# Kernel tuning notes

Measured on AMD Instinct MI355X. Metric: run time of the kernel, lower is better.

## Reference

```python
import jax, jax.numpy as jnp
import numpy as np

B, N, F = 8, 2048, 64
H, LAT = 256, 64
K1, K2 = N // 2, N // 4  # DiffPool keeps nodes//2 per stage


def _adj_mm(A, x):
    # A: [N,M] (shared) or [B,N,M] (per-sample); x: [B,M,F]
    if A.ndim == 2:
        return jnp.einsum('nm,bmf->bnf', A, x)
    return jnp.einsum('bnm,bmf->bnf', A, x)


def _gcn(x, A, W, b, act=None):
    # spektral GCNConv: act(A @ (X W) + b)
    h = _adj_mm(A, x @ W) + b
    return act(h) if act is not None else h


def _diffpool(x, A, K_emb, K_pool):
    # spektral DiffPool (linear embedding activation, softmax selection)
    z = _adj_mm(A, x @ K_emb)                               # [B,N,C]
    s = jax.nn.softmax(_adj_mm(A, x @ K_pool), axis=-1)     # [B,N,K]
    x_pool = jnp.einsum('bnk,bnc->bkc', s, z)               # S^T Z
    AS = _adj_mm(A, s)                                       # [B,N,K]
    A_pool = jnp.einsum('bnk,bnl->bkl', s, AS)              # S^T A S
    return x_pool, A_pool, s


def setup_inputs() -> dict:
    key = jax.random.key(0)
    ks = jax.random.split(key, 24)

    def glorot(k, shape):
        return (jax.random.normal(k, shape) * jnp.sqrt(2.0 / (shape[0] + shape[1]))).astype(jnp.float32)

    # symmetric sparse-ish adjacency with self loops, GCN-normalized (keeps activations stable)
    mask = (jax.random.uniform(ks[0], (N, N)) < 0.01).astype(jnp.float32)
    A = jnp.minimum(jnp.maximum(mask, mask.T) + jnp.eye(N, dtype=jnp.float32), 1.0)
    dinv = 1.0 / jnp.sqrt(jnp.sum(A, axis=-1))
    adj = A * dinv[:, None] * dinv[None, :]

    return {
        'x': jax.random.normal(ks[1], (B, N, F), dtype=jnp.float32),
        'eps': jax.random.normal(ks[2], (B, K2, LAT), dtype=jnp.float32),
        'adj': adj,
        'We1': glorot(ks[3], (F, H)), 'be1': jnp.zeros((H,), jnp.float32),
        'Kemb1': glorot(ks[4], (H, H)), 'Kpool1': glorot(ks[5], (H, K1)),
        'We2': glorot(ks[6], (H, H)), 'be2': jnp.zeros((H,), jnp.float32),
        'Kemb2': glorot(ks[7], (H, H)), 'Kpool2': glorot(ks[8], (H, K2)),
        'We3': glorot(ks[9], (H, 2 * LAT)), 'be3': jnp.zeros((2 * LAT,), jnp.float32),
        'Wd0': glorot(ks[10], (LAT, H)), 'bd0': jnp.zeros((H,), jnp.float32),
        'Wd1': glorot(ks[11], (H, H)), 'bd1': jnp.zeros((H,), jnp.float32),
        'Wd2': glorot(ks[12], (H, H)), 'bd2': jnp.zeros((H,), jnp.float32),
        'Wdf': glorot(ks[13], (H, F)), 'bdf': jnp.zeros((F,), jnp.float32),
    }


def reference(x, eps, adj, We1, be1, Kemb1, Kpool1, We2, be2, Kemb2, Kpool2,
              We3, be3, Wd0, bd0, Wd1, bd1, Wd2, bd2, Wdf, bdf):
    A0 = adj
    # ---- encode ----
    h = _gcn(x, A0, We1, be1, jax.nn.relu)              # [B,N,H]
    h, A1, s1 = _diffpool(h, A0, Kemb1, Kpool1)          # [B,K1,H], [B,K1,K1], [B,N,K1]
    h = _gcn(h, A1, We2, be2, jax.nn.relu)
    h, A2, s2 = _diffpool(h, A1, Kemb2, Kpool2)          # [B,K2,H]
    h = _gcn(h, A2, We3, be3, None)                      # [B,K2,2*LAT]
    mean, log_var = jnp.split(h, 2, axis=-1)
    z = mean + jnp.exp(0.5 * log_var) * eps              # reparameterize
    # ---- decode ----
    d = _gcn(z, A2, Wd0, bd0, jax.nn.relu)
    d = jnp.einsum('bnk,bkc->bnc', s2, d)                # DiffUnpool: S @ x
    d = _gcn(d, A1, Wd1, bd1, jax.nn.relu)
    d = jnp.einsum('bnk,bkc->bnc', s1, d)
    d = _gcn(d, A0, Wd2, bd2, jax.nn.relu)
    out = _gcn(d, A0, Wdf, bdf, jax.nn.softplus)         # [B,N,F]
    return out, mean, log_var
```

## Files before the change

### kernel.cpp

```cpp
#include <hip/hip_runtime.h>
#include <math.h>

#define BATCH 8
typedef unsigned short US;

typedef __attribute__((ext_vector_type(8))) short short8;
typedef __attribute__((ext_vector_type(4))) float f32x4;

__device__ __forceinline__ US f2b(float f) {
  union { float f; unsigned u; } v; v.f = f;
  unsigned r = v.u + 0x7fffu + ((v.u >> 16) & 1u);
  return (US)(r >> 16);
}
__device__ __forceinline__ float b2f(US h) {
  union { unsigned u; float f; } v; v.u = ((unsigned)h) << 16;
  return v.f;
}

__device__ __forceinline__ void gload16(const US* g, US* l) {
  __builtin_amdgcn_global_load_lds(
      (const __attribute__((address_space(1))) unsigned int*)g,
      (__attribute__((address_space(3))) unsigned int*)l, 16, 0, 0);
}

__device__ __forceinline__ int lidx2(int r, int ko) {
  return r * 64 + ((((ko >> 3) ^ (r & 7)) << 3));
}

template <int TN, int ACT, int OUT, bool HASBIAS>
__global__ __launch_bounds__(256) void mm_k(
    const US* __restrict__ A, const US* __restrict__ B,
    const float* __restrict__ bias, void* __restrict__ Cv, void* __restrict__ Cv2,
    int M, int N, int K, int lda, long long sA, long long sB, long long sC,
    long long sC2, int gx, int gy) {
  constexpr int JF = TN / 32;
  __shared__ US As[128 * 64];
  __shared__ US Bs[TN * 64];

  const int nb = blockIdx.x;
  const int nb2 = (nb & 7) * (gx * gy) + (nb >> 3);
  const int bx = nb2 % gx;
  const int by = (nb2 / gx) % gy;
  const int b = nb2 / (gx * gy);

  A += (long long)b * sA;
  B += (long long)b * sB;
  const int m0 = by * 128, n0 = bx * TN;
  const int t = threadIdx.x, lane = t & 63, w = t >> 6;
  const int wm = (w >> 1) * 64, wn = (w & 1) * (TN / 2);
  const int l15 = lane & 15, lg = lane >> 4;
  const int lrow = lane >> 3;
  const int gcell = (((lane & 7) ^ lrow) << 3);

  f32x4 acc[4][JF];
#pragma unroll
  for (int i = 0; i < 4; ++i)
#pragma unroll
    for (int j = 0; j < JF; ++j) acc[i][j] = (f32x4){0.f, 0.f, 0.f, 0.f};

  for (int k0 = 0; k0 < K; k0 += 64) {
#pragma unroll
    for (int i = 0; i < 4; ++i) {
      const int g = w * 4 + i;
      gload16(A + (long long)(m0 + g * 8 + lrow) * lda + k0 + gcell, &As[g * 512]);
    }
#pragma unroll
    for (int i = 0; i < TN / 32; ++i) {
      const int g = w * (TN / 32) + i;
      gload16(B + (long long)(n0 + g * 8 + lrow) * K + k0 + gcell, &Bs[g * 512]);
    }
    __syncthreads();

#pragma unroll
    for (int kk = 0; kk < 2; ++kk) {
      const int ko = kk * 32 + lg * 8;
      short8 af[4], bf[JF];
#pragma unroll
      for (int i = 0; i < 4; ++i)
        af[i] = *(const short8*)&As[lidx2(wm + i * 16 + l15, ko)];
#pragma unroll
      for (int j = 0; j < JF; ++j)
        bf[j] = *(const short8*)&Bs[lidx2(wn + j * 16 + l15, ko)];
#pragma unroll
      for (int i = 0; i < 4; ++i)
#pragma unroll
        for (int j = 0; j < JF; ++j)
          acc[i][j] = __builtin_amdgcn_mfma_f32_16x16x32_bf16(af[i], bf[j],
                                                              acc[i][j], 0, 0, 0);
    }
    __syncthreads();
  }

  const long long cb = (long long)b * sC;
  const long long cb2 = (long long)b * sC2;
#pragma unroll
  for (int fj = 0; fj < JF; ++fj) {
    const int col = n0 + wn + fj * 16 + l15;
    const float bsv = HASBIAS ? bias[col] : 0.0f;
#pragma unroll
    for (int fi = 0; fi < 4; ++fi) {
      const int row0 = m0 + wm + fi * 16 + lg * 4;
      float v[4];
#pragma unroll
      for (int e = 0; e < 4; ++e) {
        float x = acc[fi][fj][e] + bsv;
        if (ACT == 1) x = fmaxf(x, 0.0f);
        if (ACT == 2) x = (x > 20.0f) ? x : log1pf(expf(x));
        v[e] = x;
      }
      if (OUT == 1 || OUT == 3) {
        ushort4 pk;
        pk.x = f2b(v[0]); pk.y = f2b(v[1]); pk.z = f2b(v[2]); pk.w = f2b(v[3]);
        US* c2 = (OUT == 3) ? (US*)Cv2 : (US*)Cv;
        *(ushort4*)&c2[cb2 + (long long)col * M + row0] = pk;
      }
      if (OUT == 0 || OUT == 3) {
#pragma unroll
        for (int e = 0; e < 4; ++e)
          ((US*)Cv)[cb + (long long)(row0 + e) * N + col] = f2b(v[e]);
      }
      if (OUT == 2) {
#pragma unroll
        for (int e = 0; e < 4; ++e)
          ((float*)Cv)[cb + (long long)(row0 + e) * N + col] = v[e];
      }
    }
  }
}

template <int OUT>
__global__ __launch_bounds__(512, 1) void mm256_k(
    const US* __restrict__ A, const US* __restrict__ B, void* __restrict__ Cv,
    void* __restrict__ Cv2, int M, int N, int K, int lda, long long sA,
    long long sB, long long sC, long long sC2, int gx, int gy) {
  __shared__ US lds[8][8192];

  const int nb = blockIdx.x;
  const int chunk = gx * gy;
  const int nb2 = (nb & 7) * chunk + (nb >> 3);
  const int bx = nb2 % gx;
  const int by = (nb2 / gx) % gy;
  const int b = nb2 / chunk;

  const int m0 = by * 256, n0 = bx * 256;
  const int tid = threadIdx.x;
  const int lane = tid & 63, w = tid >> 6;
  const int wr = w >> 2, wc = w & 3;
  const int l15 = lane & 15, lg = lane >> 4;

  const US* Ab = A + (long long)b * sA + (long long)m0 * lda;
  const US* Bb = B + (long long)b * sB + (long long)n0 * K;
  const int NT = K >> 6;

  auto stageH = [&](int H) {
    const int s = H >> 2, h = H & 3;
    const int ab = h & 1, kk = h >> 1;
    US* reg = &lds[ab * 4 + (s & 1) * 2 + kk][0];
    const US* src = ab ? Bb : Ab;
    const int ld = ab ? K : lda;
#pragma unroll
    for (int i = 0; i < 2; ++i) {
      const int rbase = (w * 2 + i) * 16;
      const int r = rbase + (lane >> 2);
      const int csrc = (lane & 3) ^ ((r >> 1) & 3);
      gload16(src + (long long)r * ld + s * 64 + kk * 32 + csrc * 8,
              reg + rbase * 32);
    }
  };

  f32x4 acc[8][4];
#pragma unroll
  for (int m = 0; m < 8; ++m)
#pragma unroll
    for (int j = 0; j < 4; ++j) acc[m][j] = (f32x4){0.f, 0.f, 0.f, 0.f};
  short8 a4[4], b4[4];

  for (int H = 0; H < 6; ++H) stageH(H);
  asm volatile("s_waitcnt vmcnt(4)" ::: "memory");
  __builtin_amdgcn_s_barrier();

#define PH(kk_, mh_, DOH, HV, VM, tt)                                          \
  {                                                                            \
    const US* Ar = &lds[((tt) & 1) * 2 + (kk_)][0];                            \
    const US* Br = &lds[4 + ((tt) & 1) * 2 + (kk_)][0];                        \
    _Pragma("unroll") for (int i = 0; i < 4; ++i) {                            \
      const int r = wr * 128 + (mh_) * 64 + i * 16 + l15;                      \
      a4[i] = *(const short8*)&Ar[r * 32 + ((lg ^ ((r >> 1) & 3)) << 3)];      \
    }                                                                          \
    if ((mh_) == 0) {                                                          \
      _Pragma("unroll") for (int j = 0; j < 4; ++j) {                          \
        const int rr = wc * 64 + j * 16 + l15;                                 \
        b4[j] = *(const short8*)&Br[rr * 32 + ((lg ^ ((rr >> 1) & 3)) << 3)];  \
      }                                                                        \
    }                                                                          \
    if (DOH) stageH(HV);                                                       \
    if ((VM) == 1) asm volatile("s_waitcnt vmcnt(4)" ::: "memory");            \
    if ((VM) == 2) asm volatile("s_waitcnt vmcnt(0)" ::: "memory");            \
    __builtin_amdgcn_s_barrier();                                              \
    __builtin_amdgcn_s_setprio(1);                                             \
    _Pragma("unroll") for (int i = 0; i < 4; ++i)                              \
      _Pragma("unroll") for (int j = 0; j < 4; ++j)                            \
        acc[(mh_) * 4 + i][j] = __builtin_amdgcn_mfma_f32_16x16x32_bf16(       \
            a4[i], b4[j], acc[(mh_) * 4 + i][j], 0, 0, 0);                     \
    __builtin_amdgcn_s_setprio(0);                                             \
    __builtin_amdgcn_s_barrier();                                              \
  }

  int t2 = 0;
  for (; t2 < NT - 2; ++t2) {
    PH(0, 0, true, 4 * t2 + 6, 0, t2)
    PH(0, 1, true, 4 * t2 + 7, 0, t2)
    PH(1, 0, true, 4 * t2 + 8, 0, t2)
    PH(1, 1, true, 4 * t2 + 9, 1, t2)
  }
  PH(0, 0, true, 4 * (NT - 2) + 6, 0, NT - 2)
  PH(0, 1, true, 4 * (NT - 2) + 7, 0, NT - 2)
  PH(1, 0, false, 0, 0, NT - 2)
  PH(1, 1, false, 0, 2, NT - 2)
  PH(0, 0, false, 0, 0, NT - 1)
  PH(0, 1, false, 0, 0, NT - 1)
  PH(1, 0, false, 0, 0, NT - 1)
  PH(1, 1, false, 0, 0, NT - 1)
#undef PH

  const long long cb = (long long)b * sC;
  const long long cb2 = (long long)b * sC2;
#pragma unroll
  for (int j = 0; j < 4; ++j) {
    const int col = n0 + wc * 64 + j * 16 + l15;
#pragma unroll
    for (int m = 0; m < 8; ++m) {
      const int row0 = m0 + wr * 128 + m * 16 + lg * 4;
      if (OUT == 1 || OUT == 3) {
        ushort4 pk;
        pk.x = f2b(acc[m][j][0]); pk.y = f2b(acc[m][j][1]);
        pk.z = f2b(acc[m][j][2]); pk.w = f2b(acc[m][j][3]);
        US* c2 = (OUT == 3) ? (US*)Cv2 : (US*)Cv;
        *(ushort4*)&c2[cb2 + (long long)col * M + row0] = pk;
      }
      if (OUT == 0 || OUT == 3) {
#pragma unroll
        for (int e = 0; e < 4; ++e)
          ((US*)Cv)[cb + (long long)(row0 + e) * N + col] = f2b(acc[m][j][e]);
      }
    }
  }
}

template <int ACT, int OUT, bool HASBIAS>
__global__ __launch_bounds__(256) void mm64_k(
    const US* __restrict__ A, const US* __restrict__ B,
    const float* __restrict__ bias, void* __restrict__ Cv,
    int M, int N, int K, int lda, long long sA, long long sB, long long sC,
    int gx, int gy) {
  __shared__ US As[4][4096];
  __shared__ US Bs[4][4096];

  const int nb = blockIdx.x;
  const int chunk = gx * gy;
  const int nb2 = (nb & 7) * chunk + (nb >> 3);
  const int bx = nb2 % gx;
  const int by = (nb2 / gx) % gy;
  const int b = nb2 / chunk;

  const int m0 = by * 64, n0 = bx * 64;
  const int tid = threadIdx.x;
  const int lane = tid & 63, w = tid >> 6;
  const int wr = w >> 1, wc = w & 1;
  const int l15 = lane & 15, lg = lane >> 4;
  const int lrow = lane >> 3;
  const int gcell = (((lane & 7) ^ lrow) << 3);

  const US* Ag = A + (long long)b * sA + (long long)m0 * lda;
  const US* Bg = B + (long long)b * sB + (long long)n0 * K;
  const int NT = K >> 6;

  auto stage = [&](int tt) {
    US* Ad = &As[tt & 3][0];
    US* Bd = &Bs[tt & 3][0];
    const int k0 = tt * 64;
#pragma unroll
    for (int i = 0; i < 2; ++i) {
      const int g = w * 2 + i;
      const int r = g * 8 + lrow;
      gload16(Ag + (long long)r * lda + k0 + gcell, Ad + g * 512);
      gload16(Bg + (long long)r * K + k0 + gcell, Bd + g * 512);
    }
  };

  f32x4 acc[2][2];
#pragma unroll
  for (int i = 0; i < 2; ++i)
#pragma unroll
    for (int j = 0; j < 2; ++j) acc[i][j] = (f32x4){0.f, 0.f, 0.f, 0.f};

  for (int i = 0; i < 3 && i < NT; ++i) stage(i);

  for (int t = 0; t < NT; ++t) {
    if (t + 3 < NT) stage(t + 3);
    const int rem = NT - 1 - t;
    if (rem >= 3) asm volatile("s_waitcnt vmcnt(12)" ::: "memory");
    else if (rem == 2) asm volatile("s_waitcnt vmcnt(8)" ::: "memory");
    else if (rem == 1) asm volatile("s_waitcnt vmcnt(4)" ::: "memory");
    else asm volatile("s_waitcnt vmcnt(0)" ::: "memory");
    __builtin_amdgcn_s_barrier();
    const US* Ad = &As[t & 3][0];
    const US* Bd = &Bs[t & 3][0];
#pragma unroll
    for (int kk = 0; kk < 2; ++kk) {
      const int ko = kk * 32 + lg * 8;
      short8 af[2], bf[2];
      af[0] = *(const short8*)&Ad[lidx2(wr * 32 + l15, ko)];
      af[1] = *(const short8*)&Ad[lidx2(wr * 32 + 16 + l15, ko)];
      bf[0] = *(const short8*)&Bd[lidx2(wc * 32 + l15, ko)];
      bf[1] = *(const short8*)&Bd[lidx2(wc * 32 + 16 + l15, ko)];
#pragma unroll
      for (int i = 0; i < 2; ++i)
#pragma unroll
        for (int j = 0; j < 2; ++j)
          acc[i][j] = __builtin_amdgcn_mfma_f32_16x16x32_bf16(af[i], bf[j],
                                                              acc[i][j], 0, 0, 0);
    }
    __builtin_amdgcn_s_barrier();
  }

  const long long cb = (long long)b * sC;
#pragma unroll
  for (int fj = 0; fj < 2; ++fj) {
    const int col = n0 + wc * 32 + fj * 16 + l15;
    const float bsv = HASBIAS ? bias[col] : 0.0f;
#pragma unroll
    for (int fi = 0; fi < 2; ++fi) {
      const int row0 = m0 + wr * 32 + fi * 16 + lg * 4;
      float v[4];
#pragma unroll
      for (int e = 0; e < 4; ++e) {
        float x = acc[fi][fj][e] + bsv;
        if (ACT == 1) x = fmaxf(x, 0.0f);
        if (ACT == 2) x = (x > 20.0f) ? x : log1pf(expf(x));
        v[e] = x;
      }
      if (OUT == 1) {
        ushort4 pk;
        pk.x = f2b(v[0]); pk.y = f2b(v[1]); pk.z = f2b(v[2]); pk.w = f2b(v[3]);
        *(ushort4*)&((US*)Cv)[cb + (long long)col * M + row0] = pk;
      } else if (OUT == 0) {
#pragma unroll
        for (int e = 0; e < 4; ++e)
          ((US*)Cv)[cb + (long long)(row0 + e) * N + col] = f2b(v[e]);
      } else {
#pragma unroll
        for (int e = 0; e < 4; ++e)
          ((float*)Cv)[cb + (long long)(row0 + e) * N + col] = v[e];
      }
    }
  }
}

template <int RPT>
__global__ __launch_bounds__(256) void sm_partial_k(
    const US* __restrict__ x, float* __restrict__ pm, float* __restrict__ ps,
    int R, int C, long long sB, int NS) {
  const int b = blockIdx.y, blk = blockIdx.x;
  const int cpr = C >> 3;
  const int t = threadIdx.x;
  const int cslot = t & (cpr - 1);
  const int rsub = t / cpr;
  const int nsub = 256 / cpr;
  const int rowsPerBlock = R / NS;
  const int r0 = blk * rowsPerBlock + rsub * RPT;
  const US* p = x + (long long)b * sB + (long long)r0 * C + cslot * 8;
  union { uint4 v; US s[8]; } buf[RPT];
#pragma unroll
  for (int i = 0; i < RPT; ++i) buf[i].v = *(const uint4*)(p + (long long)i * C);
  float M[8], S[8];
#pragma unroll
  for (int j = 0; j < 8; ++j) M[j] = b2f(buf[0].s[j]);
#pragma unroll
  for (int i = 1; i < RPT; ++i)
#pragma unroll
    for (int j = 0; j < 8; ++j) M[j] = fmaxf(M[j], b2f(buf[i].s[j]));
#pragma unroll
  for (int j = 0; j < 8; ++j) S[j] = 0.f;
#pragma unroll
  for (int i = 0; i < RPT; ++i)
#pragma unroll
    for (int j = 0; j < 8; ++j) S[j] += __expf(b2f(buf[i].s[j]) - M[j]);
  const long long pi = (long long)(b * NS + blk) * nsub + rsub;
  float* pmo = pm + pi * C + cslot * 8;
  float* pso = ps + pi * C + cslot * 8;
  *(float4*)pmo = make_float4(M[0], M[1], M[2], M[3]);
  *(float4*)(pmo + 4) = make_float4(M[4], M[5], M[6], M[7]);
  *(float4*)pso = make_float4(S[0], S[1], S[2], S[3]);
  *(float4*)(pso + 4) = make_float4(S[4], S[5], S[6], S[7]);
}

__global__ __launch_bounds__(256) void sm_combine_k(
    const float* __restrict__ pm, const float* __restrict__ ps,
    float* __restrict__ Mf, float* __restrict__ Sinv, int C, int NP) {
  const int b = blockIdx.x, t = threadIdx.x;
  const int cpr = C >> 3;
  if (t >= cpr) return;
  const int c = t * 8;
  const float* pmB = pm + (long long)b * NP * C + c;
  const float* psB = ps + (long long)b * NP * C + c;
  float M[8], S[8];
#pragma unroll
  for (int j = 0; j < 8; ++j) { M[j] = pmB[j]; S[j] = psB[j]; }
  for (int e = 1; e < NP; ++e) {
    const float* pme = pmB + (long long)e * C;
    const float* pse = psB + (long long)e * C;
#pragma unroll
    for (int j = 0; j < 8; ++j) {
      const float m2 = pme[j], s2 = pse[j];
      const float nm = fmaxf(M[j], m2);
      S[j] = S[j] * __expf(M[j] - nm) + s2 * __expf(m2 - nm);
      M[j] = nm;
    }
  }
#pragma unroll
  for (int j = 0; j < 8; ++j) {
    Mf[(long long)b * C + c + j] = M[j];
    Sinv[(long long)b * C + c + j] = 1.0f / S[j];
  }
}

template <int RPT>
__global__ __launch_bounds__(256) void sm_norm_k(
    US* __restrict__ x, const float* __restrict__ Mf,
    const float* __restrict__ Sinv, int R, int C, long long sB, int NS) {
  const int b = blockIdx.y, blk = blockIdx.x;
  const int cpr = C >> 3;
  const int t = threadIdx.x;
  const int cslot = t & (cpr - 1);
  const int rsub = t / cpr;
  const int rowsPerBlock = R / NS;
  const int r0 = blk * rowsPerBlock + rsub * RPT;
  US* p = x + (long long)b * sB + (long long)r0 * C + cslot * 8;
  float M[8], Si[8];
#pragma unroll
  for (int j = 0; j < 8; ++j) {
    M[j] = Mf[(long long)b * C + cslot * 8 + j];
    Si[j] = Sinv[(long long)b * C + cslot * 8 + j];
  }
#pragma unroll
  for (int i = 0; i < RPT; ++i) {
    union { uint4 v; US s[8]; } buf;
    buf.v = *(const uint4*)(p + (long long)i * C);
#pragma unroll
    for (int j = 0; j < 8; ++j)
      buf.s[j] = f2b(__expf(b2f(buf.s[j]) - M[j]) * Si[j]);
    *(uint4*)(p + (long long)i * C) = buf.v;
  }
}

__global__ __launch_bounds__(256) void trans_k(const float* __restrict__ src,
                                               US* __restrict__ dst, int R, int C,
                                               long long sIn, long long sOut) {
  __shared__ US L[64][65];
  const int b = blockIdx.z;
  const int r0 = blockIdx.y * 64, c0 = blockIdx.x * 64;
  const int t = threadIdx.x;
  const int lr = t >> 4, lc = (t & 15) * 4;
  const float* s = src + (long long)b * sIn;
#pragma unroll
  for (int i = 0; i < 4; ++i) {
    const int rr = r0 + lr + 16 * i;
    const float4 v = *(const float4*)&s[(long long)rr * C + c0 + lc];
    L[lr + 16 * i][lc + 0] = f2b(v.x);
    L[lr + 16 * i][lc + 1] = f2b(v.y);
    L[lr + 16 * i][lc + 2] = f2b(v.z);
    L[lr + 16 * i][lc + 3] = f2b(v.w);
  }
  __syncthreads();
#pragma unroll
  for (int i = 0; i < 4; ++i) {
    ushort4 o;
    o.x = L[lc + 0][lr + 16 * i];
    o.y = L[lc + 1][lr + 16 * i];
    o.z = L[lc + 2][lr + 16 * i];
    o.w = L[lc + 3][lr + 16 * i];
    *(ushort4*)&dst[(long long)b * sOut + (long long)(c0 + lr + 16 * i) * R + r0 + lc] = o;
  }
}

struct WT { const float* src; US* dst; int R, C, tileOff; };
struct WTab { WT e[11]; };

__global__ __launch_bounds__(256) void wtrans_k(WTab tab) {
  __shared__ US L[64][65];
  const int tile = blockIdx.x;
  int i = 0;
#pragma unroll
  for (int j = 1; j < 11; ++j)
    if (tab.e[j].tileOff <= tile) i = j;
  const WT w = tab.e[i];
  const int lt = tile - w.tileOff;
  const int tc = w.C / 64;
  const int r0 = (lt / tc) * 64, c0 = (lt % tc) * 64;
  const int t = threadIdx.x;
  const int lr = t >> 4, lc = (t & 15) * 4;
#pragma unroll
  for (int k = 0; k < 4; ++k) {
    const int rr = r0 + lr + 16 * k;
    const float4 v = *(const float4*)&w.src[(long long)rr * w.C + c0 + lc];
    L[lr + 16 * k][lc + 0] = f2b(v.x);
    L[lr + 16 * k][lc + 1] = f2b(v.y);
    L[lr + 16 * k][lc + 2] = f2b(v.z);
    L[lr + 16 * k][lc + 3] = f2b(v.w);
  }
  __syncthreads();
#pragma unroll
  for (int k = 0; k < 4; ++k) {
    ushort4 o;
    o.x = L[lc + 0][lr + 16 * k];
    o.y = L[lc + 1][lr + 16 * k];
    o.z = L[lc + 2][lr + 16 * k];
    o.w = L[lc + 3][lr + 16 * k];
    *(ushort4*)&w.dst[(long long)(c0 + lr + 16 * k) * w.R + r0 + lc] = o;
  }
}

__global__ __launch_bounds__(256) void f2b_k(const float* __restrict__ s,
                                             US* __restrict__ d, int n4) {
  const int i = blockIdx.x * 256 + threadIdx.x;
  if (i < n4) {
    const float4 v = ((const float4*)s)[i];
    ushort4 o;
    o.x = f2b(v.x); o.y = f2b(v.y); o.z = f2b(v.z); o.w = f2b(v.w);
    ((ushort4*)d)[i] = o;
  }
}

__global__ __launch_bounds__(256) void reparam_k(
    const float* __restrict__ h3, const float* __restrict__ eps,
    float* __restrict__ om, float* __restrict__ olv, US* __restrict__ z,
    int total) {
  const int i = blockIdx.x * 256 + threadIdx.x;
  if (i >= total) return;
  const int j = i & 63;
  const long long r = i >> 6;
  const float m = h3[r * 128 + j];
  const float lv = h3[r * 128 + 64 + j];
  om[i] = m;
  olv[i] = lv;
  z[i] = f2b(m + expf(0.5f * lv) * eps[i]);
}

static void mm(hipStream_t st, const US* A, const US* B, const float* bias,
               void* C, void* C2, int M, int N, int K, int lda, long long sA,
               long long sB, long long sC, long long sC2, int act, int outm,
               int tn) {
  const int gx = N / tn, gy = M / 128;
  dim3 g(gx * gy * BATCH), blk(256);
#define L(TN, ACT, OUT, HB) \
  mm_k<TN, ACT, OUT, HB><<<g, blk, 0, st>>>(A, B, bias, C, C2, M, N, K, lda, sA, sB, sC, sC2, gx, gy)
  if (tn == 64) {
    if (outm == 0) L(64, 0, 0, false);
    else if (outm == 1) L(64, 0, 1, false);
    else L(64, 2, 2, true);
  } else {
    if (outm == 0) {
      if (act == 1) L(128, 1, 0, true);
      else L(128, 0, 0, false);
    } else if (outm == 1) {
      if (act == 1) L(128, 1, 1, true);
      else L(128, 0, 1, false);
    } else if (outm == 2) L(128, 0, 2, true);
    else L(128, 0, 3, false);
  }
#undef L
}

static void mm256(hipStream_t st, const US* A, const US* B, void* C, void* C2,
                  int M, int N, int K, int lda, long long sA, long long sB,
                  long long sC, long long sC2, int outm) {
  const int gx = N / 256, gy = M / 256;
  dim3 g(gx * gy * BATCH), blk(512);
  if (outm == 0)
    mm256_k<0><<<g, blk, 0, st>>>(A, B, C, C2, M, N, K, lda, sA, sB, sC, sC2, gx, gy);
  else if (outm == 1)
    mm256_k<1><<<g, blk, 0, st>>>(A, B, C, C2, M, N, K, lda, sA, sB, sC, sC2, gx, gy);
  else
    mm256_k<3><<<g, blk, 0, st>>>(A, B, C, C2, M, N, K, lda, sA, sB, sC, sC2, gx, gy);
}

static void mm64(hipStream_t st, const US* A, const US* B, const float* bias,
                 void* C, int M, int N, int K, int lda, long long sA,
                 long long sB, long long sC, int act, int outm) {
  const int gx = N / 64, gy = M / 64;
  dim3 g(gx * gy * BATCH), blk(256);
  if (outm == 0)
    mm64_k<0, 0, false><<<g, blk, 0, st>>>(A, B, nullptr, C, M, N, K, lda, sA, sB, sC, gx, gy);
  else if (outm == 1)
    mm64_k<0, 1, false><<<g, blk, 0, st>>>(A, B, nullptr, C, M, N, K, lda, sA, sB, sC, gx, gy);
  else
    mm64_k<2, 2, true><<<g, blk, 0, st>>>(A, B, bias, C, M, N, K, lda, sA, sB, sC, gx, gy);
}

extern "C" void kernel_launch(void* const* d_in, const int* in_sizes, int n_in,
                              void* d_out, int out_size, void* d_ws, size_t ws_size,
                              hipStream_t stream) {
  const float* x      = (const float*)d_in[0];
  const float* eps    = (const float*)d_in[1];
  const float* adj    = (const float*)d_in[2];
  const float* We1    = (const float*)d_in[3];
  const float* be1    = (const float*)d_in[4];
  const float* Kemb1  = (const float*)d_in[5];
  const float* Kpool1 = (const float*)d_in[6];
  const float* We2    = (const float*)d_in[7];
  const float* be2    = (const float*)d_in[8];
  const float* Kemb2  = (const float*)d_in[9];
  const float* Kpool2 = (const float*)d_in[10];
  const float* We3    = (const float*)d_in[11];
  const float* be3    = (const float*)d_in[12];
  const float* Wd0    = (const float*)d_in[13];
  const float* bd0    = (const float*)d_in[14];
  const float* Wd1    = (const float*)d_in[15];
  const float* bd1    = (const float*)d_in[16];
  const float* Wd2    = (const float*)d_in[17];
  const float* bd2    = (const float*)d_in[18];
  const float* Wdf    = (const float*)d_in[19];
  const float* bdf    = (const float*)d_in[20];
  (void)in_sizes; (void)n_in; (void)ws_size; (void)out_size;

  float* out = (float*)d_out;
  float* out_mean = out + (long long)8 * 2048 * 64;
  float* out_lv = out_mean + (long long)8 * 512 * 64;

  char* base = (char*)d_ws;
  size_t off = 0;
  auto alloc = [&](size_t bytes) {
    char* p = base + off;
    off += (bytes + 255) & ~(size_t)255;
    return p;
  };
  US* adjb = (US*)alloc(2048LL * 2048 * 2);
  US* xT   = (US*)alloc(8LL * 64 * 2048 * 2);
  US* Y0   = (US*)alloc(8LL * 2048 * 64 * 2);
  US* h1T  = (US*)alloc(8LL * 256 * 2048 * 2);
  US* g1   = (US*)alloc(8LL * 2048 * 256 * 2);
  US* R1   = (US*)alloc(8LL * 2304 * 2048 * 2);
  US* AS1  = (US*)alloc(8LL * 2048 * 1024 * 2);
  US* P1o  = (US*)alloc(8LL * 1024 * 1280 * 2);
  US* t1T  = (US*)alloc(8LL * 256 * 1024 * 2);
  US* h2T  = (US*)alloc(8LL * 256 * 1024 * 2);
  US* g2   = (US*)alloc(8LL * 1024 * 256 * 2);
  US* R2   = (US*)alloc(8LL * 1280 * 1024 * 2);
  US* AS2  = (US*)alloc(8LL * 1024 * 512 * 2);
  US* P2o  = (US*)alloc(8LL * 512 * 768 * 2);
  US* t2T  = (US*)alloc(8LL * 128 * 512 * 2);
  float* h3f = (float*)alloc(8LL * 512 * 128 * 4);
  US* zlb  = (US*)alloc(8LL * 512 * 64 * 2);
  US* t3T  = (US*)alloc(8LL * 256 * 512 * 2);
  US* d0   = (US*)alloc(8LL * 512 * 256 * 2);
  US* t4T  = (US*)alloc(8LL * 256 * 512 * 2);
  US* d2   = (US*)alloc(8LL * 1024 * 256 * 2);
  US* t5T  = (US*)alloc(8LL * 256 * 1024 * 2);
  US* d4   = (US*)alloc(8LL * 2048 * 256 * 2);
  US* t6T  = (US*)alloc(8LL * 64 * 2048 * 2);
  float* pm   = (float*)alloc(8LL * 128 * 2048 * 4);
  float* ps   = (float*)alloc(8LL * 128 * 2048 * 4);
  float* Mf   = (float*)alloc(8LL * 2048 * 4);
  float* Sinv = (float*)alloc(8LL * 2048 * 4);
  US* We1T  = (US*)alloc(256 * 64 * 2);
  US* KpKe1 = (US*)alloc(1280 * 256 * 2);
  US* We2T  = (US*)alloc(256 * 256 * 2);
  US* KpKe2 = (US*)alloc(768 * 256 * 2);
  US* We3T  = (US*)alloc(128 * 256 * 2);
  US* Wd0T  = (US*)alloc(256 * 64 * 2);
  US* Wd1T  = (US*)alloc(256 * 256 * 2);
  US* Wd2T  = (US*)alloc(256 * 256 * 2);
  US* WdfT  = (US*)alloc(64 * 256 * 2);

  f2b_k<<<dim3(2048 * 2048 / 4 / 256), dim3(256), 0, stream>>>(adj, adjb, 2048 * 2048 / 4);
  trans_k<<<dim3(1, 32, 8), dim3(256), 0, stream>>>(x, xT, 2048, 64, 2048LL * 64,
                                                    64LL * 2048);
  {
    WTab tab;
    int toff = 0, i = 0;
    auto add = [&](const float* s, US* d, int R, int C) {
      tab.e[i++] = WT{s, d, R, C, toff};
      toff += (R / 64) * (C / 64);
    };
    add(We1, We1T, 64, 256);
    add(Kpool1, KpKe1, 256, 1024);
    add(Kemb1, KpKe1 + 1024 * 256, 256, 256);
    add(We2, We2T, 256, 256);
    add(Kpool2, KpKe2, 256, 512);
    add(Kemb2, KpKe2 + 512 * 256, 256, 256);
    add(We3, We3T, 256, 128);
    add(Wd0, Wd0T, 64, 256);
    add(Wd1, Wd1T, 256, 256);
    add(Wd2, Wd2T, 256, 256);
    add(Wdf, WdfT, 256, 64);
    wtrans_k<<<dim3(toff), dim3(256), 0, stream>>>(tab);
  }

  const long long SR1 = 2304LL * 2048, SR2 = 1280LL * 1024;
  US* s1T  = R1;
  US* B1   = R1 + 1024 * 2048;
  US* AS1T = R1 + 1280 * 2048;
  US* s2T  = R2;
  US* B2   = R2 + 512 * 1024;
  US* AS2T = R2 + 768 * 1024;
  US* A1c  = P1o + 256;
  US* A2c  = P2o + 256;

  mm64(stream, adjb, xT, nullptr, Y0, 2048, 64, 2048, 2048, 0, 64LL * 2048,
       2048LL * 64, 0, 0);
  mm(stream, Y0, We1T, be1, h1T, nullptr, 2048, 256, 64, 64, 2048LL * 64, 0, 0,
     256LL * 2048, 1, 1, 128);
  mm(stream, adjb, h1T, nullptr, g1, nullptr, 2048, 256, 2048, 2048, 0,
     256LL * 2048, 2048LL * 256, 0, 0, 0, 128);
  mm(stream, g1, KpKe1, nullptr, R1, nullptr, 2048, 1280, 256, 256, 2048LL * 256,
     0, 0, SR1, 0, 1, 128);
  sm_partial_k<8><<<dim3(128, 8), dim3(256), 0, stream>>>(s1T, pm, ps, 1024, 2048, SR1, 128);
  sm_combine_k<<<dim3(8), dim3(256), 0, stream>>>(pm, ps, Mf, Sinv, 2048, 128);
  sm_norm_k<8><<<dim3(128, 8), dim3(256), 0, stream>>>(s1T, Mf, Sinv, 1024, 2048, SR1, 128);
  mm256(stream, adjb, s1T, AS1, AS1T, 2048, 1024, 2048, 2048, 0, SR1,
        2048LL * 1024, SR1, 3);
  mm(stream, s1T, B1, nullptr, P1o, nullptr, 1024, 1280, 2048, 2048, SR1, SR1,
     1024LL * 1280, 0, 0, 0, 128);
  mm(stream, P1o, We2T, nullptr, t1T, nullptr, 1024, 256, 256, 1280, 1024LL * 1280,
     0, 0, 256LL * 1024, 0, 1, 128);
  mm(stream, A1c, t1T, be2, h2T, nullptr, 1024, 256, 1024, 1280, 1024LL * 1280,
     256LL * 1024, 0, 256LL * 1024, 1, 1, 128);
  mm(stream, A1c, h2T, nullptr, g2, nullptr, 1024, 256, 1024, 1280, 1024LL * 1280,
     256LL * 1024, 1024LL * 256, 0, 0, 0, 128);
  mm(stream, g2, KpKe2, nullptr, R2, nullptr, 1024, 768, 256, 256, 1024LL * 256,
     0, 0, SR2, 0, 1, 128);
  sm_partial_k<4><<<dim3(64, 8), dim3(256), 0, stream>>>(s2T, pm, ps, 512, 1024, SR2, 64);
  sm_combine_k<<<dim3(8), dim3(256), 0, stream>>>(pm, ps, Mf, Sinv, 1024, 128);
  sm_norm_k<4><<<dim3(64, 8), dim3(256), 0, stream>>>(s2T, Mf, Sinv, 512, 1024, SR2, 64);
  mm(stream, A1c, s2T, nullptr, AS2, AS2T, 1024, 512, 1024, 1280, 1024LL * 1280,
     SR2, 1024LL * 512, SR2, 0, 3, 128);
  mm(stream, s2T, B2, nullptr, P2o, nullptr, 512, 768, 1024, 1024, SR2, SR2,
     512LL * 768, 0, 0, 0, 128);
  mm(stream, P2o, We3T, nullptr, t2T, nullptr, 512, 128, 256, 768, 512LL * 768,
     0, 0, 128LL * 512, 0, 1, 128);
  mm(stream, A2c, t2T, be3, h3f, nullptr, 512, 128, 512, 768, 512LL * 768,
     128LL * 512, 512LL * 128, 0, 0, 2, 128);
  reparam_k<<<dim3(8 * 512 * 64 / 256), dim3(256), 0, stream>>>(h3f, eps, out_mean,
                                                                out_lv, zlb, 8 * 512 * 64);

  mm(stream, zlb, Wd0T, nullptr, t3T, nullptr, 512, 256, 64, 64, 512LL * 64, 0, 0,
     256LL * 512, 0, 1, 128);
  mm(stream, A2c, t3T, bd0, d0, nullptr, 512, 256, 512, 768, 512LL * 768,
     256LL * 512, 512LL * 256, 0, 1, 0, 128);
  mm(stream, d0, Wd1T, nullptr, t4T, nullptr, 512, 256, 256, 256, 512LL * 256, 0,
     0, 256LL * 512, 0, 1, 128);
  mm(stream, AS2, t4T, bd1, d2, nullptr, 1024, 256, 512, 512, 1024LL * 512,
     256LL * 512, 1024LL * 256, 0, 1, 0, 128);
  mm(stream, d2, Wd2T, nullptr, t5T, nullptr, 1024, 256, 256, 256, 1024LL * 256, 0,
     0, 256LL * 1024, 0, 1, 128);
  mm(stream, AS1, t5T, bd2, d4, nullptr, 2048, 256, 1024, 1024, 2048LL * 1024,
     256LL * 1024, 2048LL * 256, 0, 1, 0, 128);
  mm64(stream, d4, WdfT, nullptr, t6T, 2048, 64, 256, 256, 2048LL * 256, 0,
       64LL * 2048, 0, 1);
  mm64(stream, adjb, t6T, bdf, out, 2048, 64, 2048, 2048, 0, 64LL * 2048,
       2048LL * 64, 2, 2);
}
```

Baseline: 664.4 us.

## Double-buffer generic GEMM, trim barriers in 256 GEMM, route big GEMMs to it

The generic mm_k kernel gets double-buffered LDS staging, so the next K-tile's global-to-LDS loads are issued while MFMAs run on the current tile. The 256-tile pipelined kernel drops several per-phase barriers and keeps only those needed for buffer reuse. Two large GEMMs, the pooling projection and S^T·B, are moved from the 128-tile kernel to the 256-tile kernel. Double buffering doubles LDS use, which may lower occupancy, and removing barriers risks LDS read/write races if the remaining ones are not enough.

Result: slower. 714.9 us (+7.6%).

```diff
diff --git a/kernel.cpp b/kernel.cpp
--- a/kernel.cpp
+++ b/kernel.cpp
@@ -34,8 +34,8 @@
     int M, int N, int K, int lda, long long sA, long long sB, long long sC,
     long long sC2, int gx, int gy) {
   constexpr int JF = TN / 32;
-  __shared__ US As[128 * 64];
-  __shared__ US Bs[TN * 64];
+  __shared__ US As[2][128 * 64];
+  __shared__ US Bs[2][TN * 64];
 
   const int nb = blockIdx.x;
   const int nb2 = (nb & 7) * (gx * gy) + (nb >> 3);
@@ -52,35 +52,43 @@
   const int lrow = lane >> 3;
   const int gcell = (((lane & 7) ^ lrow) << 3);
 
-  f32x4 acc[4][JF];
-#pragma unroll
-  for (int i = 0; i < 4; ++i)
-#pragma unroll
-    for (int j = 0; j < JF; ++j) acc[i][j] = (f32x4){0.f, 0.f, 0.f, 0.f};
-
-  for (int k0 = 0; k0 < K; k0 += 64) {
+  auto stage = [&](int buf, int k0) {
 #pragma unroll
     for (int i = 0; i < 4; ++i) {
       const int g = w * 4 + i;
-      gload16(A + (long long)(m0 + g * 8 + lrow) * lda + k0 + gcell, &As[g * 512]);
+      gload16(A + (long long)(m0 + g * 8 + lrow) * lda + k0 + gcell,
+              &As[buf][g * 512]);
     }
 #pragma unroll
     for (int i = 0; i < TN / 32; ++i) {
       const int g = w * (TN / 32) + i;
-      gload16(B + (long long)(n0 + g * 8 + lrow) * K + k0 + gcell, &Bs[g * 512]);
-    }
-    __syncthreads();
-
+      gload16(B + (long long)(n0 + g * 8 + lrow) * K + k0 + gcell,
+              &Bs[buf][g * 512]);
+    }
+  };
+
+  f32x4 acc[4][JF];
+#pragma unroll
+  for (int i = 0; i < 4; ++i)
+#pragma unroll
+    for (int j = 0; j < JF; ++j) acc[i][j] = (f32x4){0.f, 0.f, 0.f, 0.f};
+
+  stage(0, 0);
+  __syncthreads();
+
+  int cur = 0;
+  for (int k0 = 0; k0 < K; k0 += 64) {
+    if (k0 + 64 < K) stage(cur ^ 1, k0 + 64);
 #pragma unroll
     for (int kk = 0; kk < 2; ++kk) {
       const int ko = kk * 32 + lg * 8;
       short8 af[4], bf[JF];
 #pragma unroll
       for (int i = 0; i < 4; ++i)
-        af[i] = *(const short8*)&As[lidx2(wm + i * 16 + l15, ko)];
+        af[i] = *(const short8*)&As[cur][lidx2(wm + i * 16 + l15, ko)];
 #pragma unroll
       for (int j = 0; j < JF; ++j)
-        bf[j] = *(const short8*)&Bs[lidx2(wn + j * 16 + l15, ko)];
+        bf[j] = *(const short8*)&Bs[cur][lidx2(wn + j * 16 + l15, ko)];
 #pragma unroll
       for (int i = 0; i < 4; ++i)
 #pragma unroll
@@ -88,7 +96,9 @@
           acc[i][j] = __builtin_amdgcn_mfma_f32_16x16x32_bf16(af[i], bf[j],
                                                               acc[i][j], 0, 0, 0);
     }
-    __syncthreads();
+    asm volatile("s_waitcnt vmcnt(0)" ::: "memory");
+    asm volatile("s_barrier" ::: "memory");
+    cur ^= 1;
   }
 
   const long long cb = (long long)b * sC;
@@ -177,9 +187,9 @@
 
   for (int H = 0; H < 6; ++H) stageH(H);
   asm volatile("s_waitcnt vmcnt(4)" ::: "memory");
-  __builtin_amdgcn_s_barrier();
-
-#define PH(kk_, mh_, DOH, HV, VM, tt)                                          \
+  asm volatile("s_barrier" ::: "memory");
+
+#define PH(kk_, mh_, DOH, HV, VM, PB, EB, tt)                                  \
   {                                                                            \
     const US* Ar = &lds[((tt) & 1) * 2 + (kk_)][0];                            \
     const US* Br = &lds[4 + ((tt) & 1) * 2 + (kk_)][0];                        \
@@ -196,31 +206,31 @@
     if (DOH) stageH(HV);                                                       \
     if ((VM) == 1) asm volatile("s_waitcnt vmcnt(4)" ::: "memory");            \
     if ((VM) == 2) asm volatile("s_waitcnt vmcnt(0)" ::: "memory");            \
-    __builtin_amdgcn_s_barrier();                                              \
+    if (PB) asm volatile("s_barrier" ::: "memory");                            \
     __builtin_amdgcn_s_setprio(1);                                             \
     _Pragma("unroll") for (int i = 0; i < 4; ++i)                              \
       _Pragma("unroll") for (int j = 0; j < 4; ++j)                            \
         acc[(mh_) * 4 + i][j] = __builtin_amdgcn_mfma_f32_16x16x32_bf16(       \
             a4[i], b4[j], acc[(mh_) * 4 + i][j], 0, 0, 0);                     \
     __builtin_amdgcn_s_setprio(0);                                             \
-    __builtin_amdgcn_s_barrier();                                              \
+    if (EB) asm volatile("s_barrier" ::: "memory");                            \
   }
 
   int t2 = 0;
   for (; t2 < NT - 2; ++t2) {
-    PH(0, 0, true, 4 * t2 + 6, 0, t2)
-    PH(0, 1, true, 4 * t2 + 7, 0, t2)
-    PH(1, 0, true, 4 * t2 + 8, 0, t2)
-    PH(1, 1, true, 4 * t2 + 9, 1, t2)
-  }
-  PH(0, 0, true, 4 * (NT - 2) + 6, 0, NT - 2)
-  PH(0, 1, true, 4 * (NT - 2) + 7, 0, NT - 2)
-  PH(1, 0, false, 0, 0, NT - 2)
-  PH(1, 1, false, 0, 2, NT - 2)
-  PH(0, 0, false, 0, 0, NT - 1)
-  PH(0, 1, false, 0, 0, NT - 1)
-  PH(1, 0, false, 0, 0, NT - 1)
-  PH(1, 1, false, 0, 0, NT - 1)
+    PH(0, 0, true, 4 * t2 + 6, 0, 0, 0, t2)
+    PH(0, 1, true, 4 * t2 + 7, 0, 0, 1, t2)
+    PH(1, 0, true, 4 * t2 + 8, 0, 0, 0, t2)
+    PH(1, 1, true, 4 * t2 + 9, 1, 1, 1, t2)
+  }
+  PH(0, 0, true, 4 * (NT - 2) + 6, 0, 0, 0, NT - 2)
+  PH(0, 1, true, 4 * (NT - 2) + 7, 0, 0, 0, NT - 2)
+  PH(1, 0, false, 0, 0, 0, 0, NT - 2)
+  PH(1, 1, false, 0, 2, 1, 0, NT - 2)
+  PH(0, 0, false, 0, 0, 0, 0, NT - 1)
+  PH(0, 1, false, 0, 0, 0, 0, NT - 1)
+  PH(1, 0, false, 0, 0, 0, 0, NT - 1)
+  PH(1, 1, false, 0, 0, 0, 0, NT - 1)
 #undef PH
 
   const long long cb = (long long)b * sC;
@@ -303,7 +313,7 @@
     else if (rem == 2) asm volatile("s_waitcnt vmcnt(8)" ::: "memory");
     else if (rem == 1) asm volatile("s_waitcnt vmcnt(4)" ::: "memory");
     else asm volatile("s_waitcnt vmcnt(0)" ::: "memory");
-    __builtin_amdgcn_s_barrier();
+    asm volatile("s_barrier" ::: "memory");
     const US* Ad = &As[t & 3][0];
     const US* Bd = &Bs[t & 3][0];
 #pragma unroll
@@ -321,7 +331,7 @@
           acc[i][j] = __builtin_amdgcn_mfma_f32_16x16x32_bf16(af[i], bf[j],
                                                               acc[i][j], 0, 0, 0);
     }
-    __builtin_amdgcn_s_barrier();
+    asm volatile("s_barrier" ::: "memory");
   }
 
   const long long cb = (long long)b * sC;
@@ -713,15 +723,15 @@
      256LL * 2048, 1, 1, 128);
   mm(stream, adjb, h1T, nullptr, g1, nullptr, 2048, 256, 2048, 2048, 0,
      256LL * 2048, 2048LL * 256, 0, 0, 0, 128);
-  mm(stream, g1, KpKe1, nullptr, R1, nullptr, 2048, 1280, 256, 256, 2048LL * 256,
-     0, 0, SR1, 0, 1, 128);
+  mm256(stream, g1, KpKe1, R1, nullptr, 2048, 1280, 256, 256, 2048LL * 256, 0,
+        SR1, SR1, 1);
   sm_partial_k<8><<<dim3(128, 8), dim3(256), 0, stream>>>(s1T, pm, ps, 1024, 2048, SR1, 128);
   sm_combine_k<<<dim3(8), dim3(256), 0, stream>>>(pm, ps, Mf, Sinv, 2048, 128);
   sm_norm_k<8><<<dim3(128, 8), dim3(256), 0, stream>>>(s1T, Mf, Sinv, 1024, 2048, SR1, 128);
   mm256(stream, adjb, s1T, AS1, AS1T, 2048, 1024, 2048, 2048, 0, SR1,
         2048LL * 1024, SR1, 3);
-  mm(stream, s1T, B1, nullptr, P1o, nullptr, 1024, 1280, 2048, 2048, SR1, SR1,
-     1024LL * 1280, 0, 0, 0, 128);
+  mm256(stream, s1T, B1, P1o, nullptr, 1024, 1280, 2048, 2048, SR1, SR1,
+        1024LL * 1280, 0, 0);
   mm(stream, P1o, We2T, nullptr, t1T, nullptr, 1024, 256, 256, 1280, 1024LL * 1280,
      0, 0, 256LL * 1024, 0, 1, 128);
   mm(stream, A1c, t1T, be2, h2T, nullptr, 1024, 256, 1024, 1280, 1024LL * 1280,
```

## Software-pipeline LDS fragment reads in 256-tile GEMM and route more GEMMs to it

Applied to the files above, without the earlier changes.

Restructures the 256x256 GEMM main loop so that LDS fragment reads for the next phase are issued right after each barrier and overlap with the MFMAs of the current phase. This uses double-buffered A/B register fragments and removes the second barrier per phase. Two large GEMMs (the stage-1 pool/embed projection and the S^T·[Z|AS] product) are switched from the 128-tile kernel to the 256-tile kernel to get more data reuse. The cost is higher register pressure and tighter reliance on hand-placed waitcnt and barrier ordering for correctness.

After: 716.4 us. 1.08x slower.

```diff
diff --git a/kernel.cpp b/kernel.cpp
--- a/kernel.cpp
+++ b/kernel.cpp
@@ -173,55 +173,74 @@
   for (int m = 0; m < 8; ++m)
 #pragma unroll
     for (int j = 0; j < 4; ++j) acc[m][j] = (f32x4){0.f, 0.f, 0.f, 0.f};
-  short8 a4[4], b4[4];
+  short8 a0[4], a1[4], b0[4], b1[4];
+
+#define RDA(par, kk, mh, dst)                                                  \
+  {                                                                            \
+    const US* Ar_ = &lds[(par) * 2 + (kk)][0];                                 \
+    _Pragma("unroll") for (int i_ = 0; i_ < 4; ++i_) {                         \
+      const int r_ = wr * 128 + (mh) * 64 + i_ * 16 + l15;                     \
+      dst[i_] = *(const short8*)&Ar_[r_ * 32 + ((lg ^ ((r_ >> 1) & 3)) << 3)]; \
+    }                                                                          \
+  }
+#define RDB(par, kk, dst)                                                      \
+  {                                                                            \
+    const US* Br_ = &lds[4 + (par) * 2 + (kk)][0];                             \
+    _Pragma("unroll") for (int j_ = 0; j_ < 4; ++j_) {                         \
+      const int r_ = wc * 64 + j_ * 16 + l15;                                  \
+      dst[j_] = *(const short8*)&Br_[r_ * 32 + ((lg ^ ((r_ >> 1) & 3)) << 3)]; \
+    }                                                                          \
+  }
+#define MFMA16(AV, BV, MH)                                                     \
+  __builtin_amdgcn_s_setprio(1);                                               \
+  _Pragma("unroll") for (int i_ = 0; i_ < 4; ++i_)                             \
+  _Pragma("unroll") for (int j_ = 0; j_ < 4; ++j_)                             \
+      acc[(MH) * 4 + i_][j_] = __builtin_amdgcn_mfma_f32_16x16x32_bf16(        \
+          AV[i_], BV[j_], acc[(MH) * 4 + i_][j_], 0, 0, 0);                    \
+  __builtin_amdgcn_s_setprio(0);
+#define BAR asm volatile("s_barrier" ::: "memory")
+#define VMC(N) asm volatile("s_waitcnt vmcnt(" #N ")" ::: "memory")
 
   for (int H = 0; H < 6; ++H) stageH(H);
-  asm volatile("s_waitcnt vmcnt(4)" ::: "memory");
-  __builtin_amdgcn_s_barrier();
-
-#define PH(kk_, mh_, DOH, HV, VM, tt)                                          \
-  {                                                                            \
-    const US* Ar = &lds[((tt) & 1) * 2 + (kk_)][0];                            \
-    const US* Br = &lds[4 + ((tt) & 1) * 2 + (kk_)][0];                        \
-    _Pragma("unroll") for (int i = 0; i < 4; ++i) {                            \
-      const int r = wr * 128 + (mh_) * 64 + i * 16 + l15;                      \
-      a4[i] = *(const short8*)&Ar[r * 32 + ((lg ^ ((r >> 1) & 3)) << 3)];      \
-    }                                                                          \
-    if ((mh_) == 0) {                                                          \
-      _Pragma("unroll") for (int j = 0; j < 4; ++j) {                          \
-        const int rr = wc * 64 + j * 16 + l15;                                 \
-        b4[j] = *(const short8*)&Br[rr * 32 + ((lg ^ ((rr >> 1) & 3)) << 3)];  \
-      }                                                                        \
-    }                                                                          \
-    if (DOH) stageH(HV);                                                       \
-    if ((VM) == 1) asm volatile("s_waitcnt vmcnt(4)" ::: "memory");            \
-    if ((VM) == 2) asm volatile("s_waitcnt vmcnt(0)" ::: "memory");            \
-    __builtin_amdgcn_s_barrier();                                              \
-    __builtin_amdgcn_s_setprio(1);                                             \
-    _Pragma("unroll") for (int i = 0; i < 4; ++i)                              \
-      _Pragma("unroll") for (int j = 0; j < 4; ++j)                            \
-        acc[(mh_) * 4 + i][j] = __builtin_amdgcn_mfma_f32_16x16x32_bf16(       \
-            a4[i], b4[j], acc[(mh_) * 4 + i][j], 0, 0, 0);                     \
-    __builtin_amdgcn_s_setprio(0);                                             \
-    __builtin_amdgcn_s_barrier();                                              \
-  }
-
-  int t2 = 0;
-  for (; t2 < NT - 2; ++t2) {
-    PH(0, 0, true, 4 * t2 + 6, 0, t2)
-    PH(0, 1, true, 4 * t2 + 7, 0, t2)
-    PH(1, 0, true, 4 * t2 + 8, 0, t2)
-    PH(1, 1, true, 4 * t2 + 9, 1, t2)
-  }
-  PH(0, 0, true, 4 * (NT - 2) + 6, 0, NT - 2)
-  PH(0, 1, true, 4 * (NT - 2) + 7, 0, NT - 2)
-  PH(1, 0, false, 0, 0, NT - 2)
-  PH(1, 1, false, 0, 2, NT - 2)
-  PH(0, 0, false, 0, 0, NT - 1)
-  PH(0, 1, false, 0, 0, NT - 1)
-  PH(1, 0, false, 0, 0, NT - 1)
-  PH(1, 1, false, 0, 0, NT - 1)
-#undef PH
+  VMC(4);
+  BAR;
+  RDA(0, 0, 0, a0);
+  RDB(0, 0, b0);
+
+  for (int t = 0; t <= NT - 3; ++t) {
+    const int par = t & 1, npar = par ^ 1;
+    stageH(4 * t + 6);
+    BAR; RDA(par, 0, 1, a1);                      MFMA16(a0, b0, 0);
+    stageH(4 * t + 7);
+    BAR; RDA(par, 1, 0, a0); RDB(par, 1, b1);     MFMA16(a1, b0, 1);
+    stageH(4 * t + 8);
+    BAR; RDA(par, 1, 1, a1);                      MFMA16(a0, b1, 0);
+    stageH(4 * t + 9);
+    VMC(4);
+    BAR; RDA(npar, 0, 0, a0); RDB(npar, 0, b0);   MFMA16(a1, b1, 1);
+  }
+  {
+    const int par = (NT - 2) & 1, npar = par ^ 1;
+    stageH(4 * (NT - 2) + 6);
+    BAR; RDA(par, 0, 1, a1);                      MFMA16(a0, b0, 0);
+    stageH(4 * (NT - 2) + 7);
+    BAR; RDA(par, 1, 0, a0); RDB(par, 1, b1);     MFMA16(a1, b0, 1);
+    BAR; RDA(par, 1, 1, a1);                      MFMA16(a0, b1, 0);
+    VMC(0);
+    BAR; RDA(npar, 0, 0, a0); RDB(npar, 0, b0);   MFMA16(a1, b1, 1);
+  }
+  {
+    const int par = (NT - 1) & 1;
+    RDA(par, 0, 1, a1);                           MFMA16(a0, b0, 0);
+    RDA(par, 1, 0, a0); RDB(par, 1, b1);          MFMA16(a1, b0, 1);
+    RDA(par, 1, 1, a1);                           MFMA16(a0, b1, 0);
+    MFMA16(a1, b1, 1);
+  }
+#undef RDA
+#undef RDB
+#undef MFMA16
+#undef BAR
+#undef VMC
 
   const long long cb = (long long)b * sC;
   const long long cb2 = (long long)b * sC2;
@@ -303,7 +322,7 @@
     else if (rem == 2) asm volatile("s_waitcnt vmcnt(8)" ::: "memory");
     else if (rem == 1) asm volatile("s_waitcnt vmcnt(4)" ::: "memory");
     else asm volatile("s_waitcnt vmcnt(0)" ::: "memory");
-    __builtin_amdgcn_s_barrier();
+    asm volatile("s_barrier" ::: "memory");
     const US* Ad = &As[t & 3][0];
     const US* Bd = &Bs[t & 3][0];
 #pragma unroll
@@ -321,7 +340,7 @@
           acc[i][j] = __builtin_amdgcn_mfma_f32_16x16x32_bf16(af[i], bf[j],
                                                               acc[i][j], 0, 0, 0);
     }
-    __builtin_amdgcn_s_barrier();
+    asm volatile("s_barrier" ::: "memory");
   }
 
   const long long cb = (long long)b * sC;
@@ -713,15 +732,15 @@
      256LL * 2048, 1, 1, 128);
   mm(stream, adjb, h1T, nullptr, g1, nullptr, 2048, 256, 2048, 2048, 0,
      256LL * 2048, 2048LL * 256, 0, 0, 0, 128);
-  mm(stream, g1, KpKe1, nullptr, R1, nullptr, 2048, 1280, 256, 256, 2048LL * 256,
-     0, 0, SR1, 0, 1, 128);
+  mm256(stream, g1, KpKe1, R1, nullptr, 2048, 1280, 256, 256, 2048LL * 256, 0,
+        SR1, SR1, 1);
   sm_partial_k<8><<<dim3(128, 8), dim3(256), 0, stream>>>(s1T, pm, ps, 1024, 2048, SR1, 128);
   sm_combine_k<<<dim3(8), dim3(256), 0, stream>>>(pm, ps, Mf, Sinv, 2048, 128);
   sm_norm_k<8><<<dim3(128, 8), dim3(256), 0, stream>>>(s1T, Mf, Sinv, 1024, 2048, SR1, 128);
   mm256(stream, adjb, s1T, AS1, AS1T, 2048, 1024, 2048, 2048, 0, SR1,
         2048LL * 1024, SR1, 3);
-  mm(stream, s1T, B1, nullptr, P1o, nullptr, 1024, 1280, 2048, 2048, SR1, SR1,
-     1024LL * 1280, 0, 0, 0, 128);
+  mm256(stream, s1T, B1, P1o, nullptr, 1024, 1280, 2048, 2048, SR1, SR1,
+        1024LL * 1280, 0, 0);
   mm(stream, P1o, We2T, nullptr, t1T, nullptr, 1024, 256, 256, 1280, 1024LL * 1280,
      0, 0, 256LL * 1024, 0, 1, 128);
   mm(stream, A1c, t1T, be2, h2T, nullptr, 1024, 256, 1024, 1280, 1024LL * 1280,
```
